# Kernel optimization log

Hardware: AMD Instinct MI355X
Metric: run time of the kernel (lower is better)

The kernel has to match this reference:

```python
import jax, jax.numpy as jnp
import numpy as np

N, M, F_IN, F_OUT, B = 8192, 4096, 256, 128, 2048
NEG = -9e15
EPS = 1e-5


def leaky(x, slope=0.2):
    return jnp.where(x > 0, x, slope * x)


def batchnorm(x, gamma, beta):
    # BatchNorm1d training-mode semantics: biased batch stats over dim 0
    m = x.mean(axis=0)
    v = jnp.var(x, axis=0)
    return (x - m) * jax.lax.rsqrt(v + EPS) * gamma + beta


def setup_inputs() -> dict:
    key = jax.random.key(0)
    ks = jax.random.split(key, 12)
    inp = {}
    inp["Sinput"] = jax.random.normal(ks[0], (N, F_IN), dtype=jnp.float32)
    inp["Rinput"] = jax.random.normal(ks[1], (M, F_IN), dtype=jnp.float32)
    inp["inter_adj"] = jax.random.randint(ks[2], (N, M), 0, 2).astype(jnp.int32)
    inp["city_adj"] = jax.random.randint(ks[3], (N, N), 0, 2).astype(jnp.int32)
    inp["province_adj"] = jax.random.randint(ks[4], (N, N), 0, 2).astype(jnp.int32)
    inp["source_index"] = jax.random.randint(ks[5], (B,), 0, N).astype(jnp.int32)
    s_w = 1.414 * np.sqrt(6.0 / (F_IN + F_OUT))  # xavier_uniform gain=1.414
    s_a = 1.414 * np.sqrt(6.0 / (2 * F_OUT + 1))
    inp["W1"] = jax.random.uniform(ks[6], (F_IN, F_OUT), jnp.float32, -s_w, s_w)
    inp["W2"] = jax.random.uniform(ks[7], (F_IN, F_OUT), jnp.float32, -s_w, s_w)
    inp["a"] = jax.random.uniform(ks[8], (2 * F_OUT, 1), jnp.float32, -s_a, s_a)
    inp["a3"] = jax.random.uniform(ks[9], (2 * F_OUT, 1), jnp.float32, -s_a, s_a)
    inp["a4"] = jax.random.uniform(ks[10], (2 * F_OUT, 1), jnp.float32, -s_a, s_a)
    inp["bn1_gamma"] = jnp.ones((F_OUT,), jnp.float32)
    inp["bn1_beta"] = jnp.zeros((F_OUT,), jnp.float32)
    inp["bn2_gamma"] = jnp.ones((F_OUT,), jnp.float32)
    inp["bn2_beta"] = jnp.zeros((F_OUT,), jnp.float32)
    return inp


def reference(Sinput, Rinput, inter_adj, city_adj, province_adj, source_index,
              W1, W2, a, a3, a4, bn1_gamma, bn1_beta, bn2_gamma, bn2_beta):
    F = W1.shape[1]
    h1 = Rinput @ W1            # [M, F]
    h2 = Sinput @ W2            # [N, F]
    # Decomposed GAT score: cat([h1[m], h2[n]]) @ a == h1[m]@a[:F] + h2[n]@a[F:]
    e12 = leaky((h2 @ a[F:, 0])[:, None] + (h1 @ a[:F, 0])[None, :])  # [N, M]
    att_inter = jax.nn.softmax(jnp.where(inter_adj > 0, e12, NEG), axis=1)
    h2_ = h2[source_index]      # [B, F]
    # cat([h2_, h2_]) @ a3 -> h2_ @ (a3[:F] + a3[F:]), constant along N axis
    s3 = leaky(h2_ @ (a3[:F, 0] + a3[F:, 0]))  # [B]
    s4 = leaky(h2_ @ (a4[:F, 0] + a4[F:, 0]))  # [B]
    Nn = Sinput.shape[0]
    e3 = jnp.broadcast_to(s3[:, None], (s3.shape[0], Nn))
    e4 = jnp.broadcast_to(s4[:, None], (s4.shape[0], Nn))
    att3 = jax.nn.softmax(jnp.where(city_adj[source_index] > 0, e3, NEG), axis=1)
    att4 = jax.nn.softmax(jnp.where(province_adj[source_index] > 0, e4, NEG), axis=1)
    InterRC = att_inter @ h1                    # [N, F]
    IntraNC = att3.T @ h2_ + att4.T @ h2_       # [N, F]
    v_output = leaky(batchnorm(att_inter.T @ h2, bn1_gamma, bn1_beta))  # [M, F]
    u_output = leaky(batchnorm(InterRC + IntraNC, bn2_gamma, bn2_beta))  # [N, F]
    h_prime = u_output @ v_output.T             # [N, M]
    return jax.nn.elu(h_prime)
```

## Files before the change

### kernel.cpp

```cpp
#include <hip/hip_runtime.h>
#include <stdint.h>

#define N_ 8192
#define M_ 4096
#define FIN_ 256
#define F_ 128
#define B_ 2048

typedef __attribute__((ext_vector_type(8))) short vs8;
typedef __attribute__((ext_vector_type(8))) __bf16 vb8;
typedef __attribute__((ext_vector_type(4))) float vf4;

union ABu { vs8 s; vb8 b; };

__device__ __forceinline__ vf4 mfma16(const ABu& a, const ABu& b, vf4 c) {
    return __builtin_amdgcn_mfma_f32_16x16x32_bf16(a.b, b.b, c, 0, 0, 0);
}
__device__ __forceinline__ unsigned short f2b(float x) {
    union { float f; unsigned u; } v; v.f = x;
    unsigned r = v.u + 0x7fffu + ((v.u >> 16) & 1u);
    return (unsigned short)(r >> 16);
}
__device__ __forceinline__ float lrelu(float x) { return x > 0.f ? x : 0.2f * x; }

__device__ __forceinline__ void glds16(const unsigned short* g, void* l) {
    __builtin_amdgcn_global_load_lds((const __attribute__((address_space(1))) unsigned int*)g,
                                     (__attribute__((address_space(3))) unsigned int*)l, 16, 0, 0);
}

__global__ void k_prep(const float* __restrict__ W1, const float* __restrict__ W2,
                       unsigned short* __restrict__ W1T, unsigned short* __restrict__ W2T,
                       float4* __restrict__ Z, int nz4) {
    int id = blockIdx.x * 256 + threadIdx.x;
    if (id < 65536) {
        const float* W = (id < 32768) ? W1 : W2;
        unsigned short* WT = (id < 32768) ? W1T : W2T;
        int o = id & 32767;
        int f = o >> 8, k = o & 255;
        WT[o] = f2b(W[k * F_ + f]);
    } else {
        int z = id - 65536;
        if (z < nz4) Z[z] = make_float4(0.f, 0.f, 0.f, 0.f);
    }
}

__global__ __launch_bounds__(256) void k_hgemmF(const float* __restrict__ Rin, const float* __restrict__ Sin,
                                                const unsigned short* __restrict__ W1T,
                                                const unsigned short* __restrict__ W2T,
                                                const float* __restrict__ a,
                                                float* __restrict__ h2,
                                                unsigned short* __restrict__ h1P, unsigned short* __restrict__ h2P,
                                                float* __restrict__ s1, float* __restrict__ s2) {
    __shared__ unsigned short tb[16][136];
    __shared__ float sred[4][16];
    int t = threadIdx.x;
    int w = t >> 6, l = t & 63, lr = l & 15, lg = l >> 4;
    int gr = blockIdx.x * 16;
    const float* X; const unsigned short* WT; unsigned short* HP; float* sout; const float* av;
    int row0; bool isH2;
    if (gr < M_) { X = Rin; WT = W1T; HP = h1P; sout = s1; av = a;      row0 = gr;      isH2 = false; }
    else         { X = Sin; WT = W2T; HP = h2P; sout = s2; av = a + F_; row0 = gr - M_; isH2 = true;  }
    int fbase = w * 32;
    vf4 acc[2] = {};
    const float* xp = X + (size_t)(row0 + lr) * FIN_ + lg * 8;
#pragma unroll
    for (int kk = 0; kk < FIN_; kk += 32) {
        float4 xa = *(const float4*)(xp + kk);
        float4 xb = *(const float4*)(xp + kk + 4);
        ABu af;
        af.s[0] = (short)f2b(xa.x); af.s[1] = (short)f2b(xa.y);
        af.s[2] = (short)f2b(xa.z); af.s[3] = (short)f2b(xa.w);
        af.s[4] = (short)f2b(xb.x); af.s[5] = (short)f2b(xb.y);
        af.s[6] = (short)f2b(xb.z); af.s[7] = (short)f2b(xb.w);
#pragma unroll
        for (int q = 0; q < 2; ++q) {
            ABu bf; bf.s = *(const vs8*)(WT + (fbase + q * 16 + lr) * FIN_ + kk + lg * 8);
            acc[q] = mfma16(af, bf, acc[q]);
        }
    }
    if (isH2) {
#pragma unroll
        for (int q = 0; q < 2; ++q)
#pragma unroll
            for (int r = 0; r < 4; ++r)
                h2[(size_t)(row0 + lg * 4 + r) * F_ + fbase + q * 16 + lr] = acc[q][r];
    }
#pragma unroll
    for (int q = 0; q < 2; ++q)
#pragma unroll
        for (int r = 0; r < 4; ++r)
            tb[lg * 4 + r][fbase + q * 16 + lr] = f2b(acc[q][r]);
    float a0 = av[fbase + lr], a1 = av[fbase + 16 + lr];
    float tv[4];
#pragma unroll
    for (int r = 0; r < 4; ++r) tv[r] = acc[0][r] * a0 + acc[1][r] * a1;
#pragma unroll
    for (int off = 1; off < 16; off <<= 1)
#pragma unroll
        for (int r = 0; r < 4; ++r) tv[r] += __shfl_xor(tv[r], off, 64);
    if ((l & 15) == 0)
#pragma unroll
        for (int r = 0; r < 4; ++r) sred[w][lg * 4 + r] = tv[r];
    __syncthreads();
    {
        int f = t >> 1, half = t & 1;
        vs8 o;
#pragma unroll
        for (int j = 0; j < 8; ++j) o[j] = (short)tb[half * 8 + j][f];
        *(vs8*)(HP + ((size_t)(row0 >> 5) * 128 + f) * 32 + (row0 & 16) + half * 8) = o;
    }
    if (t < 16) {
        float s = sred[0][t] + sred[1][t] + sred[2][t] + sred[3][t];
        sout[row0 + t] = s;
    }
}

__global__ __launch_bounds__(256) void k_adjgather(const int* __restrict__ inter, const float* __restrict__ s1,
                                                   const float* __restrict__ s2, unsigned short* __restrict__ bm,
                                                   float* __restrict__ rowmax, float* __restrict__ rowinv,
                                                   const int* __restrict__ city, const int* __restrict__ prov,
                                                   const int* __restrict__ src,
                                                   uint32_t* __restrict__ BMtc, uint32_t* __restrict__ BMtp,
                                                   float* __restrict__ w3, float* __restrict__ w4,
                                                   const float* __restrict__ h2, unsigned short* __restrict__ h2wP) {
    __shared__ float wred[8];
    int t = threadIdx.x;
    int wv = t >> 6, ln = t & 63;
    if (blockIdx.x < N_) {
        int n = blockIdx.x;
        const int* rp = inter + (size_t)n * M_ + t * 16;
        float sv[16]; unsigned mask = 0;
#pragma unroll
        for (int c = 0; c < 4; ++c) {
            int4 v = *(const int4*)(rp + c * 4);
            if (v.x > 0) mask |= 1u << (c * 4 + 0);
            if (v.y > 0) mask |= 1u << (c * 4 + 1);
            if (v.z > 0) mask |= 1u << (c * 4 + 2);
            if (v.w > 0) mask |= 1u << (c * 4 + 3);
            float4 s = *(const float4*)(s1 + t * 16 + c * 4);
            sv[c * 4 + 0] = s.x; sv[c * 4 + 1] = s.y; sv[c * 4 + 2] = s.z; sv[c * 4 + 3] = s.w;
        }
        bm[(size_t)n * 256 + t] = (unsigned short)(mask & 0xffffu);
        float mx = -3.0e38f;
#pragma unroll
        for (int j = 0; j < 16; ++j) if (mask & (1u << j)) mx = fmaxf(mx, sv[j]);
        for (int off = 32; off > 0; off >>= 1) mx = fmaxf(mx, __shfl_down(mx, off, 64));
        if (ln == 0) wred[wv] = mx;
        __syncthreads();
        float s1mx = fmaxf(fmaxf(wred[0], wred[1]), fmaxf(wred[2], wred[3]));
        float s2n = s2[n];
        float rmx = lrelu(s2n + s1mx);
        float sum = 0.f;
#pragma unroll
        for (int j = 0; j < 16; ++j) if (mask & (1u << j)) sum += __expf(lrelu(s2n + sv[j]) - rmx);
        for (int off = 32; off > 0; off >>= 1) sum += __shfl_down(sum, off, 64);
        if (ln == 0) wred[4 + wv] = sum;
        __syncthreads();
        if (t == 0) {
            float tot = wred[4] + wred[5] + wred[6] + wred[7];
            bool any = s1mx > -2.9e38f;
            rowmax[n] = any ? rmx : 0.f;
            rowinv[n] = (any && tot > 0.f) ? 1.0f / tot : 0.f;
        }
    } else if (blockIdx.x < N_ + 2 * B_) {
        int bb = blockIdx.x - N_;
        int b = bb & (B_ - 1);
        bool isC = bb < B_;
        const int* adj = isC ? city : prov;
        uint32_t* BM = isC ? BMtc : BMtp;
        float* wout = isC ? w3 : w4;
        const int* rowp = adj + (size_t)src[b] * N_;
        int cnt = 0;
#pragma unroll 4
        for (int i = 0; i < N_ / 256; ++i) {
            int v = rowp[i * 256 + t];
            unsigned long long bal = __ballot(v > 0);
            cnt += (v > 0);
            if (ln == 0) {
                int widx = i * 8 + wv * 2;
                BM[(size_t)widx * B_ + b] = (uint32_t)bal;
                BM[(size_t)(widx + 1) * B_ + b] = (uint32_t)(bal >> 32);
            }
        }
        float fc = (float)cnt;
        for (int off = 32; off > 0; off >>= 1) fc += __shfl_down(fc, off, 64);
        if (ln == 0) wred[wv] = fc;
        __syncthreads();
        if (t == 0) {
            float tot = wred[0] + wred[1] + wred[2] + wred[3];
            wout[b] = tot > 0.f ? 1.0f / tot : 0.f;
        }
    } else {
        int bblk = blockIdx.x - (N_ + 2 * B_);
        int f = t & 127, halfb = t >> 7;
        vs8 o0, o1;
#pragma unroll
        for (int i = 0; i < 8; ++i) {
            int b0 = bblk * 32 + halfb * 16 + i;
            o0[i] = (short)f2b(h2[(size_t)src[b0] * F_ + f]);
            int b1 = b0 + 8;
            o1[i] = (short)f2b(h2[(size_t)src[b1] * F_ + f]);
        }
        unsigned short* dst = h2wP + ((size_t)bblk * 128 + f) * 32 + halfb * 16;
        *(vs8*)dst = o0;
        *(vs8*)(dst + 8) = o1;
    }
}

__global__ __launch_bounds__(256) void k_attmat2(const unsigned char* __restrict__ bm8,
                                                 const float* __restrict__ s1, const float* __restrict__ s2,
                                                 const float* __restrict__ rowmax, const float* __restrict__ rowinv,
                                                 unsigned short* __restrict__ attP,
                                                 unsigned short* __restrict__ attT) {
    __shared__ unsigned short tile[64][33];
    int bx = blockIdx.x;
    int mt = bx & 63, nt = bx >> 6;
    int nb = nt * 32, mb = mt * 64;
    int t = threadIdx.x;
    int mo = t & 7, nl = t >> 3;
    int n = nb + nl;
    int m = mb + mo * 8;
    unsigned bits = bm8[(size_t)n * 512 + (m >> 3)];
    float s2n = s2[n], rmx = rowmax[n], rin = rowinv[n];
    float4 sa = *(const float4*)(s1 + m);
    float4 sb = *(const float4*)(s1 + m + 4);
    float sv[8] = {sa.x, sa.y, sa.z, sa.w, sb.x, sb.y, sb.z, sb.w};
    vs8 o;
#pragma unroll
    for (int j = 0; j < 8; ++j) {
        float v = (bits & (1u << j)) ? __expf(lrelu(s2n + sv[j]) - rmx) * rin : 0.f;
        o[j] = (short)f2b(v);
        tile[mo * 8 + j][nl] = (unsigned short)o[j];
    }
    *(vs8*)(attP + ((size_t)(m >> 5) * N_ + n) * 32 + (m & 31)) = o;
    __syncthreads();
    int mr = t >> 2, sg = t & 3;
    vs8 ot;
#pragma unroll
    for (int j = 0; j < 8; ++j) ot[j] = (short)tile[mr][sg * 8 + j];
    *(vs8*)(attT + ((size_t)nt * M_ + mb + mr) * 32 + sg * 8) = ot;
}

__global__ __launch_bounds__(256) void k_gemmABC(const unsigned short* __restrict__ attP,
                                                 const unsigned short* __restrict__ attT,
                                                 const unsigned short* __restrict__ h1P,
                                                 const unsigned short* __restrict__ h2P,
                                                 const uint32_t* __restrict__ BMtc, const uint32_t* __restrict__ BMtp,
                                                 const float* __restrict__ w3, const float* __restrict__ w4,
                                                 const unsigned short* __restrict__ h2wP,
                                                 float* __restrict__ uP, float* __restrict__ vP) {
    __shared__ __align__(16) unsigned short smem[16384];
    int t = threadIdx.x;
    int w = t >> 6, l = t & 63;
    int lr = l & 15, lg = l >> 4;
    int bx = blockIdx.x;
    if (bx < 384) {
        bool isA = bx < 256;
        int i = isA ? bx : bx - 256;
        int x, y, ns, kbase, rowsK;
        const unsigned short* Asrc; const unsigned short* Bsrc; float* Out;
        if (isA) { x = i & 63; y = i >> 6; ns = 32; kbase = y * 32; rowsK = N_;
                   Asrc = attP; Bsrc = h1P; Out = uP + (size_t)y * N_ * F_; }
        else     { x = i & 31; y = i >> 5; ns = 64; kbase = y * 64; rowsK = M_;
                   Asrc = attT; Bsrc = h2P; Out = vP + (size_t)y * M_ * F_; }
        int rb0 = x * 128;
        int rq = (w >> 1) * 64;
        int cb = (w & 1) * 64;
        auto stage = [&](int kb, int buf) {
#pragma unroll
            for (int ii = 0; ii < 4; ++ii) {
                int c = w * 4 + ii;
                const unsigned short* g; int loff;
                if (c < 8) { g = Asrc + ((size_t)kb * rowsK + rb0) * 32 + c * 512 + l * 8;
                             loff = buf * 8192 + c * 512; }
                else       { g = Bsrc + (size_t)kb * 4096 + (c - 8) * 512 + l * 8;
                             loff = buf * 8192 + 4096 + (c - 8) * 512; }
                glds16(g, smem + loff);
            }
        };
        vf4 acc[4][4] = {};
        stage(kbase, 0);
        __syncthreads();
        int cur = 0;
        for (int step = 0; step < ns; ++step) {
            if (step + 1 < ns) stage(kbase + step + 1, cur ^ 1);
            const unsigned short* base = smem + cur * 8192;
            ABu a[4], b[4];
#pragma unroll
            for (int s = 0; s < 4; ++s) a[s].s = *(const vs8*)(base + (rq + s * 16 + lr) * 32 + lg * 8);
#pragma unroll
            for (int q = 0; q < 4; ++q) b[q].s = *(const vs8*)(base + 4096 + (cb + q * 16 + lr) * 32 + lg * 8);
#pragma unroll
            for (int s = 0; s < 4; ++s)
#pragma unroll
                for (int q = 0; q < 4; ++q) acc[s][q] = mfma16(a[s], b[q], acc[s][q]);
            __syncthreads();
            cur ^= 1;
        }
#pragma unroll
        for (int s = 0; s < 4; ++s)
#pragma unroll
            for (int q = 0; q < 4; ++q)
#pragma unroll
                for (int r = 0; r < 4; ++r)
                    Out[(size_t)(rb0 + rq + s * 16 + lg * 4 + r) * F_ + cb + q * 16 + lr] = acc[s][q][r];
    } else {
        int i = bx - 384;
        int xc = i & 127, yc = i >> 7;
        int nb0 = xc * 64 + (w & 1) * 32;
        int fb = (w >> 1) * 64;
        int wi = nb0 >> 5;
        const uint32_t* bc = BMtc + (size_t)wi * B_;
        const uint32_t* bp = BMtp + (size_t)wi * B_;
        vf4 acc[2][4] = {};
        int b0s = yc * (B_ / 2);
        for (int b0 = b0s; b0 < b0s + B_ / 2; b0 += 32) {
            int bb = b0 + lg * 8;
            uint4 c0 = *(const uint4*)(bc + bb);
            uint4 c1 = *(const uint4*)(bc + bb + 4);
            uint4 p0 = *(const uint4*)(bp + bb);
            uint4 p1 = *(const uint4*)(bp + bb + 4);
            float4 wa = *(const float4*)(w3 + bb);
            float4 wb = *(const float4*)(w3 + bb + 4);
            float4 wc = *(const float4*)(w4 + bb);
            float4 wd = *(const float4*)(w4 + bb + 4);
            const unsigned short* hb = h2wP + (size_t)(b0 >> 5) * 128 * 32;
            ABu bf0, bf1, bf2, bf3;
            bf0.s = *(const vs8*)(hb + (size_t)(fb + lr) * 32 + lg * 8);
            bf1.s = *(const vs8*)(hb + (size_t)(fb + 16 + lr) * 32 + lg * 8);
            bf2.s = *(const vs8*)(hb + (size_t)(fb + 32 + lr) * 32 + lg * 8);
            bf3.s = *(const vs8*)(hb + (size_t)(fb + 48 + lr) * 32 + lg * 8);
            uint32_t cw[8] = {c0.x, c0.y, c0.z, c0.w, c1.x, c1.y, c1.z, c1.w};
            uint32_t pw[8] = {p0.x, p0.y, p0.z, p0.w, p1.x, p1.y, p1.z, p1.w};
            float w3v[8] = {wa.x, wa.y, wa.z, wa.w, wb.x, wb.y, wb.z, wb.w};
            float w4v[8] = {wc.x, wc.y, wc.z, wc.w, wd.x, wd.y, wd.z, wd.w};
            ABu af0, af1;
#pragma unroll
            for (int j = 0; j < 8; ++j) {
                float v0 = (((cw[j] >> lr) & 1u) ? w3v[j] : 0.f) + (((pw[j] >> lr) & 1u) ? w4v[j] : 0.f);
                float v1 = (((cw[j] >> (16 + lr)) & 1u) ? w3v[j] : 0.f) + (((pw[j] >> (16 + lr)) & 1u) ? w4v[j] : 0.f);
                af0.s[j] = (short)f2b(v0);
                af1.s[j] = (short)f2b(v1);
            }
            acc[0][0] = mfma16(af0, bf0, acc[0][0]);
            acc[1][0] = mfma16(af1, bf0, acc[1][0]);
            acc[0][1] = mfma16(af0, bf1, acc[0][1]);
            acc[1][1] = mfma16(af1, bf1, acc[1][1]);
            acc[0][2] = mfma16(af0, bf2, acc[0][2]);
            acc[1][2] = mfma16(af1, bf2, acc[1][2]);
            acc[0][3] = mfma16(af0, bf3, acc[0][3]);
            acc[1][3] = mfma16(af1, bf3, acc[1][3]);
        }
        float* Out = uP + (size_t)(4 + yc) * N_ * F_;
#pragma unroll
        for (int s = 0; s < 2; ++s)
#pragma unroll
            for (int q = 0; q < 4; ++q)
#pragma unroll
                for (int r = 0; r < 4; ++r)
                    Out[(size_t)(nb0 + s * 16 + lg * 4 + r) * F_ + fb + q * 16 + lr] = acc[s][q][r];
    }
}

__global__ __launch_bounds__(256) void k_bnstats3(const float* __restrict__ vP, const float* __restrict__ uP,
                                                  float* __restrict__ stats) {
    __shared__ float r1[256], r2[256];
    int bx = blockIdx.x;
    int f = threadIdx.x & 127;
    int half = threadIdx.x >> 7;
    float s = 0.f, s2v = 0.f;
    if (bx < 256) {
        size_t stride = (size_t)M_ * F_;
        for (int r = bx * 2 + half; r < M_; r += 512) {
            float v = 0.f;
#pragma unroll
            for (int y = 0; y < 4; ++y) v += vP[(size_t)y * stride + (size_t)r * F_ + f];
            s += v; s2v += v * v;
        }
        r1[threadIdx.x] = s; r2[threadIdx.x] = s2v;
        __syncthreads();
        if (half == 0) {
            atomicAdd(&stats[f], r1[f] + r1[f + 128]);
            atomicAdd(&stats[128 + f], r2[f] + r2[f + 128]);
        }
    } else {
        int b = bx - 256;
        size_t stride = (size_t)N_ * F_;
        for (int r = b * 2 + half; r < N_; r += 512) {
            float v = 0.f;
#pragma unroll
            for (int y = 0; y < 6; ++y) v += uP[(size_t)y * stride + (size_t)r * F_ + f];
            s += v; s2v += v * v;
        }
        r1[threadIdx.x] = s; r2[threadIdx.x] = s2v;
        __syncthreads();
        if (half == 0) {
            atomicAdd(&stats[256 + f], r1[f] + r1[f + 128]);
            atomicAdd(&stats[384 + f], r2[f] + r2[f + 128]);
        }
    }
}

__global__ __launch_bounds__(256) void k_bnapplyP(const float* __restrict__ vP, const float* __restrict__ uP,
                                                  const float* __restrict__ stats,
                                                  const float* __restrict__ g1, const float* __restrict__ b1,
                                                  const float* __restrict__ g2, const float* __restrict__ b2,
                                                  unsigned short* __restrict__ v_outb, unsigned short* __restrict__ u_outb) {
    __shared__ float sc[256], sh[256];
    int t = threadIdx.x;
    {
        int which = t >> 7, f = t & 127;
        const float* sum = stats + which * 256;
        const float* sq = sum + 128;
        const float* g = which ? g2 : g1;
        const float* be = which ? b2 : b1;
        float R = which ? (float)N_ : (float)M_;
        float mean = sum[f] / R;
        float var = sq[f] / R - mean * mean;
        float s = g[f] * rsqrtf(var + 1e-5f);
        sc[t] = s; sh[t] = be[f] - mean * s;
    }
    __syncthreads();
    int id4 = blockIdx.x * 256 + t;
    int idx = id4 * 4;
    int which = idx >= M_ * F_;
    int rel = which ? idx - M_ * F_ : idx;
    int f0 = (rel & 127) + which * 128;
    float4 p = make_float4(0.f, 0.f, 0.f, 0.f);
    unsigned short* Q;
    if (!which) {
        size_t stride = (size_t)M_ * F_;
#pragma unroll
        for (int y = 0; y < 4; ++y) {
            float4 q = *(const float4*)(vP + (size_t)y * stride + rel);
            p.x += q.x; p.y += q.y; p.z += q.z; p.w += q.w;
        }
        Q = v_outb;
    } else {
        size_t stride = (size_t)N_ * F_;
#pragma unroll
        for (int y = 0; y < 6; ++y) {
            float4 q = *(const float4*)(uP + (size_t)y * stride + rel);
            p.x += q.x; p.y += q.y; p.z += q.z; p.w += q.w;
        }
        Q = u_outb;
    }
    ushort4 o;
    o.x = f2b(lrelu(p.x * sc[f0 + 0] + sh[f0 + 0]));
    o.y = f2b(lrelu(p.y * sc[f0 + 1] + sh[f0 + 1]));
    o.z = f2b(lrelu(p.z * sc[f0 + 2] + sh[f0 + 2]));
    o.w = f2b(lrelu(p.w * sc[f0 + 3] + sh[f0 + 3]));
    *(ushort4*)(Q + rel) = o;
}

__global__ __launch_bounds__(256) void k_gemmD(const unsigned short* __restrict__ U,
                                               const unsigned short* __restrict__ V,
                                               float* __restrict__ out) {
    int w = threadIdx.x >> 6, l = threadIdx.x & 63;
    int lr = l & 15, lg = l >> 4;
    int nb = blockIdx.x * 64 + w * 16;
    int mb = blockIdx.y * 64;
    vf4 acc[4] = {};
#pragma unroll
    for (int k0 = 0; k0 < F_; k0 += 32) {
        ABu af; af.s = *(const vs8*)(U + (size_t)(nb + lr) * F_ + k0 + lg * 8);
#pragma unroll
        for (int q = 0; q < 4; ++q) {
            ABu bf; bf.s = *(const vs8*)(V + (size_t)(mb + q * 16 + lr) * F_ + k0 + lg * 8);
            acc[q] = mfma16(af, bf, acc[q]);
        }
    }
#pragma unroll
    for (int q = 0; q < 4; ++q)
#pragma unroll
        for (int r = 0; r < 4; ++r) {
            int row = nb + lg * 4 + r;
            int col = mb + q * 16 + lr;
            float x = acc[q][r];
            out[(size_t)row * M_ + col] = x > 0.f ? x : __expf(x) - 1.f;
        }
}

extern "C" void kernel_launch(void* const* d_in, const int* in_sizes, int n_in,
                              void* d_out, int out_size, void* d_ws, size_t ws_size,
                              hipStream_t stream) {
    const float* Sinput = (const float*)d_in[0];
    const float* Rinput = (const float*)d_in[1];
    const int* inter_adj = (const int*)d_in[2];
    const int* city_adj = (const int*)d_in[3];
    const int* prov_adj = (const int*)d_in[4];
    const int* src = (const int*)d_in[5];
    const float* W1 = (const float*)d_in[6];
    const float* W2 = (const float*)d_in[7];
    const float* a = (const float*)d_in[8];
    const float* g1 = (const float*)d_in[11];
    const float* b1 = (const float*)d_in[12];
    const float* g2 = (const float*)d_in[13];
    const float* b2 = (const float*)d_in[14];
    float* out = (float*)d_out;

    char* ws = (char*)d_ws;
    size_t o = 0;
    auto take = [&](size_t bytes) { char* p = ws + o; o += (bytes + 255) & ~(size_t)255; return p; };
    float* stats = (float*)take(512 * 4);
    size_t zero_bytes = o;
    float* uP = (float*)take((size_t)6 * N_ * F_ * 4);
    float* vP = (float*)take((size_t)4 * M_ * F_ * 4);
    float* h2 = (float*)take((size_t)N_ * F_ * 4);
    unsigned short* h1P = (unsigned short*)take((size_t)(M_ / 32) * 128 * 32 * 2);
    unsigned short* h2P = (unsigned short*)take((size_t)(N_ / 32) * 128 * 32 * 2);
    unsigned short* W1T = (unsigned short*)take((size_t)F_ * FIN_ * 2);
    unsigned short* W2T = (unsigned short*)take((size_t)F_ * FIN_ * 2);
    float* s1 = (float*)take(M_ * 4);
    float* s2 = (float*)take(N_ * 4);
    float* rowmax = (float*)take(N_ * 4);
    float* rowinv = (float*)take(N_ * 4);
    float* w3 = (float*)take(B_ * 4);
    float* w4 = (float*)take(B_ * 4);
    unsigned short* h2wP = (unsigned short*)take((size_t)(B_ / 32) * 128 * 32 * 2);
    unsigned short* u_outb = (unsigned short*)take((size_t)N_ * F_ * 2);
    unsigned short* v_outb = (unsigned short*)take((size_t)M_ * F_ * 2);
    uint32_t* BMtc = (uint32_t*)take((size_t)256 * B_ * 4);
    uint32_t* BMtp = (uint32_t*)take((size_t)256 * B_ * 4);
    unsigned short* bm = (unsigned short*)take((size_t)N_ * 256 * 2);
    unsigned short* attP = (unsigned short*)take((size_t)N_ * M_ * 2);
    unsigned short* attT = (unsigned short*)take((size_t)N_ * M_ * 2);
    (void)ws_size; (void)in_sizes; (void)n_in; (void)out_size;

    int nz4 = (int)(zero_bytes / 16);
    int zblocks = (nz4 + 255) / 256;
    k_prep<<<256 + zblocks, 256, 0, stream>>>(W1, W2, W1T, W2T, (float4*)d_ws, nz4);
    k_hgemmF<<<(M_ + N_) / 16, 256, 0, stream>>>(Rinput, Sinput, W1T, W2T, a, h2, h1P, h2P, s1, s2);
    k_adjgather<<<N_ + 2 * B_ + B_ / 32, 256, 0, stream>>>(inter_adj, s1, s2, bm, rowmax, rowinv,
                                                           city_adj, prov_adj, src, BMtc, BMtp, w3, w4,
                                                           h2, h2wP);
    k_attmat2<<<16384, 256, 0, stream>>>((const unsigned char*)bm, s1, s2, rowmax, rowinv, attP, attT);
    k_gemmABC<<<640, 256, 0, stream>>>(attP, attT, h1P, h2P, BMtc, BMtp, w3, w4, h2wP, uP, vP);
    k_bnstats3<<<512, 256, 0, stream>>>(vP, uP, stats);
    k_bnapplyP<<<(M_ + N_) * F_ / 4 / 256, 256, 0, stream>>>(vP, uP, stats, g1, b1, g2, b2, v_outb, u_outb);
    k_gemmD<<<dim3(N_ / 64, M_ / 64), 256, 0, stream>>>(u_outb, v_outb, out);
}
```

Baseline: 322.3 us.

## Regenerate attention tiles on the fly inside GEMM instead of materializing them

```diff
diff --git a/kernel.cpp b/kernel.cpp
--- a/kernel.cpp
+++ b/kernel.cpp
@@ -207,49 +207,33 @@
     }
 }
 
-__global__ __launch_bounds__(256) void k_attmat2(const unsigned char* __restrict__ bm8,
+__global__ __launch_bounds__(256) void k_bitT(const unsigned long long* __restrict__ bm64,
+                                              unsigned long long* __restrict__ bmT64) {
+    int tile = blockIdx.x * 4 + (threadIdx.x >> 6);
+    int l = threadIdx.x & 63;
+    int tn = tile >> 6, tm = tile & 63;
+    unsigned long long row = bm64[(size_t)(tn * 64 + l) * 64 + tm];
+    unsigned long long mine = 0;
+#pragma unroll
+    for (int c = 0; c < 64; ++c) {
+        unsigned long long b = __ballot((unsigned)((row >> c) & 1ull));
+        if (l == c) mine = b;
+    }
+    bmT64[(size_t)(tm * 64 + l) * 128 + tn] = mine;
+}
+
+__global__ __launch_bounds__(256) void k_gemmABC(const uint32_t* __restrict__ bm32,
+                                                 const uint32_t* __restrict__ bmT32,
                                                  const float* __restrict__ s1, const float* __restrict__ s2,
                                                  const float* __restrict__ rowmax, const float* __restrict__ rowinv,
-                                                 unsigned short* __restrict__ attP,
-                                                 unsigned short* __restrict__ attT) {
-    __shared__ unsigned short tile[64][33];
-    int bx = blockIdx.x;
-    int mt = bx & 63, nt = bx >> 6;
-    int nb = nt * 32, mb = mt * 64;
-    int t = threadIdx.x;
-    int mo = t & 7, nl = t >> 3;
-    int n = nb + nl;
-    int m = mb + mo * 8;
-    unsigned bits = bm8[(size_t)n * 512 + (m >> 3)];
-    float s2n = s2[n], rmx = rowmax[n], rin = rowinv[n];
-    float4 sa = *(const float4*)(s1 + m);
-    float4 sb = *(const float4*)(s1 + m + 4);
-    float sv[8] = {sa.x, sa.y, sa.z, sa.w, sb.x, sb.y, sb.z, sb.w};
-    vs8 o;
-#pragma unroll
-    for (int j = 0; j < 8; ++j) {
-        float v = (bits & (1u << j)) ? __expf(lrelu(s2n + sv[j]) - rmx) * rin : 0.f;
-        o[j] = (short)f2b(v);
-        tile[mo * 8 + j][nl] = (unsigned short)o[j];
-    }
-    *(vs8*)(attP + ((size_t)(m >> 5) * N_ + n) * 32 + (m & 31)) = o;
-    __syncthreads();
-    int mr = t >> 2, sg = t & 3;
-    vs8 ot;
-#pragma unroll
-    for (int j = 0; j < 8; ++j) ot[j] = (short)tile[mr][sg * 8 + j];
-    *(vs8*)(attT + ((size_t)nt * M_ + mb + mr) * 32 + sg * 8) = ot;
-}
-
-__global__ __launch_bounds__(256) void k_gemmABC(const unsigned short* __restrict__ attP,
-                                                 const unsigned short* __restrict__ attT,
                                                  const unsigned short* __restrict__ h1P,
                                                  const unsigned short* __restrict__ h2P,
                                                  const uint32_t* __restrict__ BMtc, const uint32_t* __restrict__ BMtp,
                                                  const float* __restrict__ w3, const float* __restrict__ w4,
                                                  const unsigned short* __restrict__ h2wP,
                                                  float* __restrict__ uP, float* __restrict__ vP) {
-    __shared__ __align__(16) unsigned short smem[16384];
+    __shared__ __align__(16) unsigned short ldsA[2][4096];
+    __shared__ __align__(16) unsigned short ldsB[2][4096];
     int t = threadIdx.x;
     int w = t >> 6, l = t & 63;
     int lr = l & 15, lg = l >> 4;
@@ -257,43 +241,85 @@
     if (bx < 384) {
         bool isA = bx < 256;
         int i = isA ? bx : bx - 256;
-        int x, y, ns, kbase, rowsK;
-        const unsigned short* Asrc; const unsigned short* Bsrc; float* Out;
-        if (isA) { x = i & 63; y = i >> 6; ns = 32; kbase = y * 32; rowsK = N_;
-                   Asrc = attP; Bsrc = h1P; Out = uP + (size_t)y * N_ * F_; }
-        else     { x = i & 31; y = i >> 5; ns = 64; kbase = y * 64; rowsK = M_;
-                   Asrc = attT; Bsrc = h2P; Out = vP + (size_t)y * M_ * F_; }
+        int x, y, ns, kbase;
+        const unsigned short* Bsrc; float* Out;
+        if (isA) { x = i & 63; y = i >> 6; ns = 32; kbase = y * 32;
+                   Bsrc = h1P; Out = uP + (size_t)y * N_ * F_; }
+        else     { x = i & 31; y = i >> 5; ns = 64; kbase = y * 64;
+                   Bsrc = h2P; Out = vP + (size_t)y * M_ * F_; }
         int rb0 = x * 128;
         int rq = (w >> 1) * 64;
         int cb = (w & 1) * 64;
-        auto stage = [&](int kb, int buf) {
-#pragma unroll
-            for (int ii = 0; ii < 4; ++ii) {
-                int c = w * 4 + ii;
-                const unsigned short* g; int loff;
-                if (c < 8) { g = Asrc + ((size_t)kb * rowsK + rb0) * 32 + c * 512 + l * 8;
-                             loff = buf * 8192 + c * 512; }
-                else       { g = Bsrc + (size_t)kb * 4096 + (c - 8) * 512 + l * 8;
-                             loff = buf * 8192 + 4096 + (c - 8) * 512; }
-                glds16(g, smem + loff);
+        int rrow = t >> 2, oct = t & 3;
+        auto regen = [&](int kb, int buf) {
+            unsigned short* dst = ldsA[buf] + rrow * 32 + oct * 8;
+            if (isA) {
+                float4 sa = *(const float4*)(s1 + kb * 32 + oct * 8);
+                float4 sb = *(const float4*)(s1 + kb * 32 + oct * 8 + 4);
+                float sv[8] = {sa.x, sa.y, sa.z, sa.w, sb.x, sb.y, sb.z, sb.w};
+#pragma unroll
+                for (int uu = 0; uu < 2; ++uu) {
+                    int n = rb0 + rrow + uu * 64;
+                    uint32_t bits = bm32[(size_t)n * 128 + kb] >> (oct * 8);
+                    float s2n = s2[n], rmx = rowmax[n], rin = rowinv[n];
+                    vs8 o;
+#pragma unroll
+                    for (int j = 0; j < 8; ++j) {
+                        float v = ((bits >> j) & 1u) ? __expf(lrelu(s2n + sv[j]) - rmx) * rin : 0.f;
+                        o[j] = (short)f2b(v);
+                    }
+                    *(vs8*)(dst + uu * 2048) = o;
+                }
+            } else {
+                float4 za = *(const float4*)(s2 + kb * 32 + oct * 8);
+                float4 zb = *(const float4*)(s2 + kb * 32 + oct * 8 + 4);
+                float4 ra = *(const float4*)(rowmax + kb * 32 + oct * 8);
+                float4 rb2 = *(const float4*)(rowmax + kb * 32 + oct * 8 + 4);
+                float4 ia = *(const float4*)(rowinv + kb * 32 + oct * 8);
+                float4 ib = *(const float4*)(rowinv + kb * 32 + oct * 8 + 4);
+                float zv[8] = {za.x, za.y, za.z, za.w, zb.x, zb.y, zb.z, zb.w};
+                float rv[8] = {ra.x, ra.y, ra.z, ra.w, rb2.x, rb2.y, rb2.z, rb2.w};
+                float iv[8] = {ia.x, ia.y, ia.z, ia.w, ib.x, ib.y, ib.z, ib.w};
+#pragma unroll
+                for (int uu = 0; uu < 2; ++uu) {
+                    int m = rb0 + rrow + uu * 64;
+                    uint32_t bits = bmT32[(size_t)m * 256 + kb] >> (oct * 8);
+                    float s1m = s1[m];
+                    vs8 o;
+#pragma unroll
+                    for (int j = 0; j < 8; ++j) {
+                        float v = ((bits >> j) & 1u) ? __expf(lrelu(zv[j] + s1m) - rv[j]) * iv[j] : 0.f;
+                        o[j] = (short)f2b(v);
+                    }
+                    *(vs8*)(dst + uu * 2048) = o;
+                }
+            }
+        };
+        auto stageB = [&](int kb, int buf) {
+#pragma unroll
+            for (int ii = 0; ii < 2; ++ii) {
+                int c = w * 2 + ii;
+                glds16(Bsrc + (size_t)kb * 4096 + c * 512 + l * 8, ldsB[buf] + c * 512);
             }
         };
         vf4 acc[4][4] = {};
-        stage(kbase, 0);
+        regen(kbase, 0);
+        stageB(kbase, 0);
         __syncthreads();
         int cur = 0;
         for (int step = 0; step < ns; ++step) {
-            if (step + 1 < ns) stage(kbase + step + 1, cur ^ 1);
-            const unsigned short* base = smem + cur * 8192;
+            int kb = kbase + step;
+            if (step + 1 < ns) stageB(kb + 1, cur ^ 1);
             ABu a[4], b[4];
 #pragma unroll
-            for (int s = 0; s < 4; ++s) a[s].s = *(const vs8*)(base + (rq + s * 16 + lr) * 32 + lg * 8);
-#pragma unroll
-            for (int q = 0; q < 4; ++q) b[q].s = *(const vs8*)(base + 4096 + (cb + q * 16 + lr) * 32 + lg * 8);
+            for (int s = 0; s < 4; ++s) a[s].s = *(const vs8*)(ldsA[cur] + (rq + s * 16 + lr) * 32 + lg * 8);
+#pragma unroll
+            for (int q = 0; q < 4; ++q) b[q].s = *(const vs8*)(ldsB[cur] + (cb + q * 16 + lr) * 32 + lg * 8);
 #pragma unroll
             for (int s = 0; s < 4; ++s)
 #pragma unroll
                 for (int q = 0; q < 4; ++q) acc[s][q] = mfma16(a[s], b[q], acc[s][q]);
+            if (step + 1 < ns) regen(kb + 1, cur ^ 1);
             __syncthreads();
             cur ^= 1;
         }
@@ -523,8 +549,7 @@
     uint32_t* BMtc = (uint32_t*)take((size_t)256 * B_ * 4);
     uint32_t* BMtp = (uint32_t*)take((size_t)256 * B_ * 4);
     unsigned short* bm = (unsigned short*)take((size_t)N_ * 256 * 2);
-    unsigned short* attP = (unsigned short*)take((size_t)N_ * M_ * 2);
-    unsigned short* attT = (unsigned short*)take((size_t)N_ * M_ * 2);
+    unsigned short* bmT = (unsigned short*)take((size_t)M_ * 512 * 2);
     (void)ws_size; (void)in_sizes; (void)n_in; (void)out_size;
 
     int nz4 = (int)(zero_bytes / 16);
@@ -534,8 +559,10 @@
     k_adjgather<<<N_ + 2 * B_ + B_ / 32, 256, 0, stream>>>(inter_adj, s1, s2, bm, rowmax, rowinv,
                                                            city_adj, prov_adj, src, BMtc, BMtp, w3, w4,
                                                            h2, h2wP);
-    k_attmat2<<<16384, 256, 0, stream>>>((const unsigned char*)bm, s1, s2, rowmax, rowinv, attP, attT);
-    k_gemmABC<<<640, 256, 0, stream>>>(attP, attT, h1P, h2P, BMtc, BMtp, w3, w4, h2wP, uP, vP);
+    k_bitT<<<2048, 256, 0, stream>>>((const unsigned long long*)bm, (unsigned long long*)bmT);
+    k_gemmABC<<<640, 256, 0, stream>>>((const uint32_t*)bm, (const uint32_t*)bmT,
+                                       s1, s2, rowmax, rowinv, h1P, h2P,
+                                       BMtc, BMtp, w3, w4, h2wP, uP, vP);
     k_bnstats3<<<512, 256, 0, stream>>>(vP, uP, stats);
     k_bnapplyP<<<(M_ + N_) * F_ / 4 / 256, 256, 0, stream>>>(vP, uP, stats, g1, b1, g2, b2, v_outb, u_outb);
     k_gemmD<<<dim3(N_ / 64, M_ / 64), 256, 0, stream>>>(u_outb, v_outb, out);
```

Result: slower. 356.0 us (+10.5%).
